# Kernel tuning notes

Measured on AMD Instinct MI355X. Metric: run time of the kernel, lower is better.

## Reference

```python
import jax, jax.numpy as jnp
import numpy as np

N_NODES = 100000
N_EDGES = 1000000
D_IN = 128
D_OUT = 128
ALPHA = 0.5


def setup_inputs() -> dict:
    key = jax.random.key(0)
    k = jax.random.split(key, 8)
    x = jax.random.normal(k[0], (N_NODES, D_IN), dtype=jnp.float32)
    edge_src = jax.random.randint(k[1], (N_EDGES,), 0, N_NODES, dtype=jnp.int32)
    edge_dst = jax.random.randint(k[2], (N_EDGES,), 0, N_NODES, dtype=jnp.int32)
    s = 1.0 / np.sqrt(D_IN)
    W_sd = jax.random.uniform(k[3], (D_OUT, D_IN), jnp.float32, -s, s)
    b_sd = jax.random.uniform(k[4], (D_OUT,), jnp.float32, -s, s)
    W_ds = jax.random.uniform(k[5], (D_OUT, D_IN), jnp.float32, -s, s)
    b_ds = jax.random.uniform(k[6], (D_OUT,), jnp.float32, -s, s)
    return {"x": x, "edge_src": edge_src, "edge_dst": edge_dst,
            "W_sd": W_sd, "b_sd": b_sd, "W_ds": W_ds, "b_ds": b_ds}


def reference(x, edge_src, edge_dst, W_sd, b_sd, W_ds, b_ds):
    # adj[dst, src] = 1 for each edge.
    # adj @ x      : aggregate source features into destination rows.
    # adj.T @ x    : aggregate destination features into source rows.
    agg_sd = jax.ops.segment_sum(x[edge_src], edge_dst, num_segments=N_NODES)  # [N, D_IN]
    agg_ds = jax.ops.segment_sum(x[edge_dst], edge_src, num_segments=N_NODES)  # [N, D_IN]
    src_to_dst = agg_sd @ W_sd.T + b_sd  # torch Linear: x W^T + b
    dst_to_src = agg_ds @ W_ds.T + b_ds
    return ALPHA * src_to_dst + (1.0 - ALPHA) * dst_to_src
```

## Files before the change

kernel.cpp:

```cpp
#include <hip/hip_runtime.h>

#define NN 100000
#define NE 1000000
#define D 128
#define ALPHA 0.5f

#define OFF_W2     102400000UL
#define OFF_BIAS   102531072UL
#define OFF_CNT    102531584UL
#define OFF_START  102931584UL
#define OFF_BINC   103331584UL
#define OFF_BINB   103333632UL
#define OFF_BINCUR 103335680UL
#define OFF_BUF    103337728UL
#define OFF_REC    111337728UL

#define NB  391
#define EPB 2048

__global__ __launch_bounds__(256) void build_w2b(const float* __restrict__ Wsd,
                                                 const float* __restrict__ Wds,
                                                 const float* __restrict__ bsd,
                                                 const float* __restrict__ bds,
                                                 float* __restrict__ W2,
                                                 float* __restrict__ bias) {
    int idx = blockIdx.x * 256 + threadIdx.x;
    int k = idx >> 7;
    int j = idx & 127;
    float v;
    if (k < 128) v = ALPHA * Wsd[j * D + k];
    else         v = (1.0f - ALPHA) * Wds[j * D + (k - 128)];
    W2[idx] = v;
    if (idx < 128) bias[idx] = ALPHA * bsd[idx] + (1.0f - ALPHA) * bds[idx];
}

__global__ __launch_bounds__(512) void zero_bins(int* __restrict__ binCnt) {
    int i = threadIdx.x;
    if (i < NB) binCnt[i] = 0;
}

__global__ __launch_bounds__(256) void count_bins(const int* __restrict__ esrc,
                                                  const int* __restrict__ edst,
                                                  int* __restrict__ binCnt) {
    __shared__ int h[NB];
    int t = threadIdx.x;
    for (int i = t; i < NB; i += 256) h[i] = 0;
    __syncthreads();
    int e0 = blockIdx.x * EPB;
    for (int i = t; i < EPB; i += 256) {
        int e = e0 + i;
        if (e < NE) {
            atomicAdd(&h[edst[e] >> 8], 1);
            atomicAdd(&h[esrc[e] >> 8], 1);
        }
    }
    __syncthreads();
    for (int i = t; i < NB; i += 256)
        if (h[i]) atomicAdd(&binCnt[i], h[i]);
}

__global__ __launch_bounds__(256) void scan_bins(const int* __restrict__ binCnt,
                                                 int* __restrict__ binBase,
                                                 int* __restrict__ binCursor) {
    __shared__ int v[NB];
    int t = threadIdx.x;
    for (int i = t; i < NB; i += 256) v[i] = binCnt[i];
    __syncthreads();
    if (t == 0) {
        int acc = 0;
        for (int i = 0; i < NB; ++i) { int c = v[i]; v[i] = acc; acc += c; }
    }
    __syncthreads();
    for (int i = t; i < NB; i += 256) { binBase[i] = v[i]; binCursor[i] = v[i]; }
}

__global__ __launch_bounds__(256) void place_bins(const int* __restrict__ esrc,
                                                  const int* __restrict__ edst,
                                                  int* __restrict__ binCursor,
                                                  int* __restrict__ rec4) {
    __shared__ int h[NB];
    __shared__ int base[NB];
    __shared__ int lcur[NB];
    int t = threadIdx.x;
    for (int i = t; i < NB; i += 256) h[i] = 0;
    __syncthreads();
    int e0 = blockIdx.x * EPB;
    for (int i = t; i < EPB; i += 256) {
        int e = e0 + i;
        if (e < NE) {
            atomicAdd(&h[edst[e] >> 8], 1);
            atomicAdd(&h[esrc[e] >> 8], 1);
        }
    }
    __syncthreads();
    for (int i = t; i < NB; i += 256) {
        if (h[i]) base[i] = atomicAdd(&binCursor[i], h[i]);
        lcur[i] = 0;
    }
    __syncthreads();
    for (int i = t; i < EPB; i += 256) {
        int e = e0 + i;
        if (e < NE) {
            int s = esrc[e], d = edst[e];
            int bd = d >> 8, bs = s >> 8;
            int p1 = atomicAdd(&lcur[bd], 1);
            rec4[base[bd] + p1] = ((d & 255) << 18) | (s << 1);
            int p2 = atomicAdd(&lcur[bs], 1);
            rec4[base[bs] + p2] = ((s & 255) << 18) | (d << 1) | 1;
        }
    }
}

__global__ __launch_bounds__(256) void build_csr(const int* __restrict__ rec4,
                                                 const int* __restrict__ binBase,
                                                 const int* __restrict__ binCnt,
                                                 int* __restrict__ buf,
                                                 int* __restrict__ start,
                                                 int* __restrict__ cnt_out) {
    __shared__ int hc[256];
    __shared__ int st[256];
    int b = blockIdx.x;
    int t = threadIdx.x;
    int node0 = b << 8;
    int r0 = binBase[b];
    int rn = binCnt[b];

    hc[t] = 0;
    __syncthreads();
    for (int i = t; i < rn; i += 256)
        atomicAdd(&hc[rec4[r0 + i] >> 18], 1);
    __syncthreads();
    if (t == 0) {
        int acc = 0;
        for (int i = 0; i < 256; ++i) { st[i] = acc; acc += hc[i]; }
    }
    __syncthreads();
    int n = node0 + t;
    if (n < NN) {
        start[n]   = r0 + st[t];
        cnt_out[n] = hc[t];
    }
    hc[t] = st[t];
    __syncthreads();
    for (int i = t; i < rn; i += 256) {
        int r = rec4[r0 + i];
        int pos = atomicAdd(&hc[r >> 18], 1);
        buf[r0 + pos] = r & 0x3FFFF;
    }
}

__global__ __launch_bounds__(256) void gather_z(const int* __restrict__ start,
                                                const int* __restrict__ cnt,
                                                const int* __restrict__ buf,
                                                const float* __restrict__ x,
                                                float* __restrict__ z) {
    int wave = blockIdx.x * 4 + (threadIdx.x >> 6);
    int lane = threadIdx.x & 63;
    if (wave >= NN) return;
    const int s0 = start[wave];
    const int e0 = s0 + cnt[wave];
    const int l2 = lane << 1;

    float a0 = 0.f, a1 = 0.f;
    float b0 = 0.f, b1 = 0.f;

#define ACCUM(v, p) if ((v) & 1) { b0 += (p).x; b1 += (p).y; } \
                    else         { a0 += (p).x; a1 += (p).y; }

    int i = s0;
    for (; i + 4 <= e0; i += 4) {
        int v0 = buf[i], v1 = buf[i + 1], v2 = buf[i + 2], v3 = buf[i + 3];
        float2 p0 = *(const float2*)&x[(size_t)(v0 >> 1) * D + l2];
        float2 p1 = *(const float2*)&x[(size_t)(v1 >> 1) * D + l2];
        float2 p2 = *(const float2*)&x[(size_t)(v2 >> 1) * D + l2];
        float2 p3 = *(const float2*)&x[(size_t)(v3 >> 1) * D + l2];
        ACCUM(v0, p0) ACCUM(v1, p1) ACCUM(v2, p2) ACCUM(v3, p3)
    }
    for (; i < e0; ++i) {
        int v0 = buf[i];
        float2 p0 = *(const float2*)&x[(size_t)(v0 >> 1) * D + l2];
        ACCUM(v0, p0)
    }
#undef ACCUM

    *(float2*)&z[(size_t)wave * 256 + l2]       = make_float2(a0, a1);
    *(float2*)&z[(size_t)wave * 256 + 128 + l2] = make_float2(b0, b1);
}

__global__ __launch_bounds__(256) void transform_z(const float* __restrict__ z,
                                                   const float* __restrict__ W2,
                                                   const float* __restrict__ bias,
                                                   float* __restrict__ out) {
    const int tid  = threadIdx.x;
    const int brow = blockIdx.x * 64;
    const int ty   = tid >> 4;
    const int tx   = tid & 15;
    const int c0   = tx << 2;

    float acc[4][2][4];
#pragma unroll
    for (int i = 0; i < 4; ++i)
#pragma unroll
        for (int g = 0; g < 2; ++g)
#pragma unroll
            for (int c = 0; c < 4; ++c) acc[i][g][c] = 0.f;

    size_t zbase[4];
    int    rvalid[4];
#pragma unroll
    for (int i = 0; i < 4; ++i) {
        int row = brow + ty * 4 + i;
        rvalid[i] = (row < NN);
        zbase[i]  = (size_t)(rvalid[i] ? row : 0) * 256;
    }

#pragma unroll 2
    for (int k0 = 0; k0 < 256; k0 += 4) {
        float4 av[4];
#pragma unroll
        for (int i = 0; i < 4; ++i)
            av[i] = *(const float4*)&z[zbase[i] + k0];
#pragma unroll
        for (int j = 0; j < 4; ++j) {
            float4 q0 = *(const float4*)&W2[(k0 + j) * 128 + c0];
            float4 q1 = *(const float4*)&W2[(k0 + j) * 128 + 64 + c0];
#pragma unroll
            for (int i = 0; i < 4; ++i) {
                float a = (&av[i].x)[j];
                acc[i][0][0] += a * q0.x; acc[i][0][1] += a * q0.y;
                acc[i][0][2] += a * q0.z; acc[i][0][3] += a * q0.w;
                acc[i][1][0] += a * q1.x; acc[i][1][1] += a * q1.y;
                acc[i][1][2] += a * q1.z; acc[i][1][3] += a * q1.w;
            }
        }
    }

    float4 bb0 = *(const float4*)&bias[c0];
    float4 bb1 = *(const float4*)&bias[64 + c0];
#pragma unroll
    for (int i = 0; i < 4; ++i) {
        if (!rvalid[i]) continue;
        int row = brow + ty * 4 + i;
        float4 o0 = make_float4(acc[i][0][0] + bb0.x, acc[i][0][1] + bb0.y,
                                acc[i][0][2] + bb0.z, acc[i][0][3] + bb0.w);
        float4 o1 = make_float4(acc[i][1][0] + bb1.x, acc[i][1][1] + bb1.y,
                                acc[i][1][2] + bb1.z, acc[i][1][3] + bb1.w);
        *(float4*)&out[(size_t)row * D + c0]      = o0;
        *(float4*)&out[(size_t)row * D + 64 + c0] = o1;
    }
}

extern "C" void kernel_launch(void* const* d_in, const int* in_sizes, int n_in,
                              void* d_out, int out_size, void* d_ws, size_t ws_size,
                              hipStream_t stream) {
    const float* x    = (const float*)d_in[0];
    const int*   esrc = (const int*)  d_in[1];
    const int*   edst = (const int*)  d_in[2];
    const float* Wsd  = (const float*)d_in[3];
    const float* bsd  = (const float*)d_in[4];
    const float* Wds  = (const float*)d_in[5];
    const float* bds  = (const float*)d_in[6];
    float* out = (float*)d_out;

    char*  ws       = (char*)d_ws;
    float* z        = (float*)ws;
    float* W2       = (float*)(ws + OFF_W2);
    float* bias     = (float*)(ws + OFF_BIAS);
    int*   cnt      = (int*)(ws + OFF_CNT);
    int*   start    = (int*)(ws + OFF_START);
    int*   binCnt   = (int*)(ws + OFF_BINC);
    int*   binBase  = (int*)(ws + OFF_BINB);
    int*   binCursor= (int*)(ws + OFF_BINCUR);
    int*   buf      = (int*)(ws + OFF_BUF);
    int*   rec4     = (int*)(ws + OFF_REC);

    const int nblk = (NE + EPB - 1) / EPB;

    build_w2b<<<128, 256, 0, stream>>>(Wsd, Wds, bsd, bds, W2, bias);
    zero_bins<<<1, 512, 0, stream>>>(binCnt);
    count_bins<<<nblk, 256, 0, stream>>>(esrc, edst, binCnt);
    scan_bins<<<1, 256, 0, stream>>>(binCnt, binBase, binCursor);
    place_bins<<<nblk, 256, 0, stream>>>(esrc, edst, binCursor, rec4);
    build_csr<<<NB, 256, 0, stream>>>(rec4, binBase, binCnt, buf, start, cnt);
    gather_z<<<(NN + 3) / 4, 256, 0, stream>>>(start, cnt, buf, x, z);
    transform_z<<<(NN + 63) / 64, 256, 0, stream>>>(z, W2, bias, out);
}
```

Baseline: 473.1 us.

## Stage z tiles in shared memory and split output columns across grid

The transform GEMM now loads each 64x128 half of the z row block cooperatively into LDS with coalesced float4 loads, then computes a 64x64 output tile per block. A second grid dimension splits the 128 output columns. Before, each thread read z rows directly with strided float4 loads. The change aims to improve coalescing of z reads and lower register use (16 accumulators instead of 32), which should raise occupancy. The cost is that z is read twice, once per column block, and the kernel gains shared-memory syncs.

```diff
diff --git a/kernel.cpp b/kernel.cpp
--- a/kernel.cpp
+++ b/kernel.cpp
@@ -191,62 +191,65 @@
                                                    const float* __restrict__ W2,
                                                    const float* __restrict__ bias,
                                                    float* __restrict__ out) {
+    __shared__ float As[64][132];
     const int tid  = threadIdx.x;
     const int brow = blockIdx.x * 64;
+    const int bcol = blockIdx.y * 64;
     const int ty   = tid >> 4;
     const int tx   = tid & 15;
-    const int c0   = tx << 2;
-
-    float acc[4][2][4];
+
+    float acc[4][4];
 #pragma unroll
     for (int i = 0; i < 4; ++i)
 #pragma unroll
-        for (int g = 0; g < 2; ++g)
-#pragma unroll
-            for (int c = 0; c < 4; ++c) acc[i][g][c] = 0.f;
-
-    size_t zbase[4];
-    int    rvalid[4];
+        for (int j = 0; j < 4; ++j) acc[i][j] = 0.f;
+
+    for (int kp = 0; kp < 2; ++kp) {
+#pragma unroll
+        for (int i = 0; i < 8; ++i) {
+            int f   = tid + i * 256;
+            int row = f >> 5;
+            int kc  = (f & 31) << 2;
+            float4 g = make_float4(0.f, 0.f, 0.f, 0.f);
+            int grow = brow + row;
+            if (grow < NN) g = *(const float4*)&z[(size_t)grow * 256 + kp * 128 + kc];
+            *(float4*)&As[row][kc] = g;
+        }
+        __syncthreads();
+
+#pragma unroll 2
+        for (int k0 = 0; k0 < 128; k0 += 4) {
+            float av[4][4], bv[4][4];
+#pragma unroll
+            for (int i = 0; i < 4; ++i) {
+                float4 t = *(const float4*)&As[ty * 4 + i][k0];
+                av[i][0] = t.x; av[i][1] = t.y; av[i][2] = t.z; av[i][3] = t.w;
+            }
+#pragma unroll
+            for (int j = 0; j < 4; ++j) {
+                float4 t = *(const float4*)&W2[(size_t)(kp * 128 + k0 + j) * 128 + bcol + tx * 4];
+                bv[j][0] = t.x; bv[j][1] = t.y; bv[j][2] = t.z; bv[j][3] = t.w;
+            }
+#pragma unroll
+            for (int i = 0; i < 4; ++i)
+#pragma unroll
+                for (int c = 0; c < 4; ++c)
+#pragma unroll
+                    for (int kk = 0; kk < 4; ++kk)
+                        acc[i][c] += av[i][kk] * bv[kk][c];
+        }
+        __syncthreads();
+    }
+
+    float4 bb = *(const float4*)&bias[bcol + tx * 4];
 #pragma unroll
     for (int i = 0; i < 4; ++i) {
         int row = brow + ty * 4 + i;
-        rvalid[i] = (row < NN);
-        zbase[i]  = (size_t)(rvalid[i] ? row : 0) * 256;
-    }
-
-#pragma unroll 2
-    for (int k0 = 0; k0 < 256; k0 += 4) {
-        float4 av[4];
-#pragma unroll
-        for (int i = 0; i < 4; ++i)
-            av[i] = *(const float4*)&z[zbase[i] + k0];
-#pragma unroll
-        for (int j = 0; j < 4; ++j) {
-            float4 q0 = *(const float4*)&W2[(k0 + j) * 128 + c0];
-            float4 q1 = *(const float4*)&W2[(k0 + j) * 128 + 64 + c0];
-#pragma unroll
-            for (int i = 0; i < 4; ++i) {
-                float a = (&av[i].x)[j];
-                acc[i][0][0] += a * q0.x; acc[i][0][1] += a * q0.y;
-                acc[i][0][2] += a * q0.z; acc[i][0][3] += a * q0.w;
-                acc[i][1][0] += a * q1.x; acc[i][1][1] += a * q1.y;
-                acc[i][1][2] += a * q1.z; acc[i][1][3] += a * q1.w;
-            }
-        }
-    }
-
-    float4 bb0 = *(const float4*)&bias[c0];
-    float4 bb1 = *(const float4*)&bias[64 + c0];
-#pragma unroll
-    for (int i = 0; i < 4; ++i) {
-        if (!rvalid[i]) continue;
-        int row = brow + ty * 4 + i;
-        float4 o0 = make_float4(acc[i][0][0] + bb0.x, acc[i][0][1] + bb0.y,
-                                acc[i][0][2] + bb0.z, acc[i][0][3] + bb0.w);
-        float4 o1 = make_float4(acc[i][1][0] + bb1.x, acc[i][1][1] + bb1.y,
-                                acc[i][1][2] + bb1.z, acc[i][1][3] + bb1.w);
-        *(float4*)&out[(size_t)row * D + c0]      = o0;
-        *(float4*)&out[(size_t)row * D + 64 + c0] = o1;
+        if (row < NN) {
+            float4 v = make_float4(acc[i][0] + bb.x, acc[i][1] + bb.y,
+                                   acc[i][2] + bb.z, acc[i][3] + bb.w);
+            *(float4*)&out[(size_t)row * D + bcol + tx * 4] = v;
+        }
     }
 }
 
@@ -283,5 +286,5 @@
     place_bins<<<nblk, 256, 0, stream>>>(esrc, edst, binCursor, rec4);
     build_csr<<<NB, 256, 0, stream>>>(rec4, binBase, binCnt, buf, start, cnt);
     gather_z<<<(NN + 3) / 4, 256, 0, stream>>>(start, cnt, buf, x, z);
-    transform_z<<<(NN + 63) / 64, 256, 0, stream>>>(z, W2, bias, out);
-}
+    transform_z<<<dim3((NN + 63) / 64, 2), 256, 0, stream>>>(z, W2, bias, out);
+}
```

Result: faster. 428.3 us (-9.5%).
